# Kernel optimization log

Hardware: AMD Instinct MI355X
Metric: run time of the kernel (lower is better)

Reference implementation:

```python
import jax, jax.numpy as jnp
import numpy as np
from jax import lax

B = 16           # graphs per batch
N_PER = 4096     # points per graph (equal-sized graphs)
C_IN = 32        # in_channels
RATIO = 0.25
MAX_NBR = 32     # max_num_neighbors in radius()


def _xavier(key, fan_in, fan_out):
    lim = np.sqrt(6.0 / (fan_in + fan_out)).astype(np.float32)
    return jax.random.uniform(key, (fan_in, fan_out), jnp.float32, -lim, lim)


def setup_inputs() -> dict:
    key = jax.random.key(0)
    ks = jax.random.split(key, 16)
    x = jax.random.normal(ks[0], (B * N_PER, C_IN), jnp.float32)
    pos = jax.random.uniform(ks[1], (B * N_PER, 3), jnp.float32) * 20.0
    batch = jnp.repeat(jnp.arange(B, dtype=jnp.int64), N_PER)
    p = {
        'x': x, 'pos': pos, 'batch': batch,
        'scaler_mean': jnp.zeros((1, C_IN), jnp.float32),
        'scaler_std': jnp.ones((1, C_IN), jnp.float32),
        # SA1: Linear(32+3,64) -> Sigmoid -> Linear(64,128)
        'sa1_w1': _xavier(ks[2], C_IN + 3, 64), 'sa1_b1': jnp.zeros((64,), jnp.float32),
        'sa1_w2': _xavier(ks[3], 64, 128),      'sa1_b2': jnp.zeros((128,), jnp.float32),
        # SA2: Linear(128+3,128) -> Sigmoid -> Linear(128,256)
        'sa2_w1': _xavier(ks[4], 128 + 3, 128), 'sa2_b1': jnp.zeros((128,), jnp.float32),
        'sa2_w2': _xavier(ks[5], 128, 256),     'sa2_b2': jnp.zeros((256,), jnp.float32),
        # Global SA: Linear(256+3,256) -> Sigmoid -> Linear(256,512)
        'g_w1': _xavier(ks[6], 256 + 3, 256),   'g_b1': jnp.zeros((256,), jnp.float32),
        'g_w2': _xavier(ks[7], 256, 512),       'g_b2': jnp.zeros((512,), jnp.float32),
        # fc: Linear(512,256) -> Sigmoid -> Linear(256,128)
        'fc_w1': _xavier(ks[8], 512, 256),      'fc_b1': jnp.zeros((256,), jnp.float32),
        'fc_w2': _xavier(ks[9], 256, 128),      'fc_b2': jnp.zeros((128,), jnp.float32),
    }
    return p


def _fps(pos, k):
    # Farthest point sampling, deterministic start at index 0. pos: [B, n, 3] -> idx [B, k]
    pos = lax.stop_gradient(pos)
    d0 = jnp.sum((pos - pos[:, :1, :]) ** 2, -1)  # [B, n] dist^2 to start point

    def step(mind, _):
        nxt = jnp.argmax(mind, axis=1)                                  # [B]
        p = jnp.take_along_axis(pos, nxt[:, None, None], axis=1)        # [B,1,3]
        mind = jnp.minimum(mind, jnp.sum((pos - p) ** 2, -1))
        return mind, nxt

    _, rest = lax.scan(step, d0, None, length=k - 1)                    # [k-1, B]
    start = jnp.zeros((1, pos.shape[0]), rest.dtype)
    return jnp.concatenate([start, rest], 0).T                          # [B, k]


def _gather_nbr(v, nbr):
    # v: [B, n, C], nbr: [B, k, MAX_NBR] -> [B, k, MAX_NBR, C]
    return jax.vmap(lambda vb, nb: vb[nb])(v, nbr)


def _sa_module(x, pos, w1, b1, w2, b2, ratio, r):
    # PointNetConv (max aggregation) over a radius graph from FPS centers.
    Bb, n, _ = x.shape
    k = int(n * ratio)
    idx = _fps(pos, k)                                                  # [B, k]
    pos_dst = jnp.take_along_axis(pos, idx[:, :, None], axis=1)         # [B, k, 3]
    d2 = jnp.sum((pos_dst[:, :, None, :] - pos[:, None, :, :]) ** 2, -1)  # [B,k,n]
    masked = jnp.where(d2 <= r * r, d2, jnp.inf)
    negv, nbr = lax.top_k(-masked, MAX_NBR)                             # nearest <=32 within radius
    valid = jnp.isfinite(negv)                                          # [B,k,32]
    x_j = _gather_nbr(x, nbr)                                           # [B,k,32,C]
    rel = _gather_nbr(pos, nbr) - pos_dst[:, :, None, :]                # pos_j - pos_i
    feat = jnp.concatenate([x_j, rel], axis=-1)
    msg = jax.nn.sigmoid(feat @ w1 + b1) @ w2 + b2                      # [B,k,32,2h]
    msg = jnp.where(valid[..., None], msg, -jnp.inf)
    agg = jnp.max(msg, axis=2)                                          # max aggregation
    agg = jnp.where(jnp.isfinite(agg), agg, 0.0)  # (self is always a neighbor, defensive)
    return jax.nn.relu(agg), pos_dst


def reference(x, pos, batch, scaler_mean, scaler_std,
              sa1_w1, sa1_b1, sa1_w2, sa1_b2,
              sa2_w1, sa2_b1, sa2_w2, sa2_b2,
              g_w1, g_b1, g_w2, g_b2,
              fc_w1, fc_b1, fc_w2, fc_b2):
    x = (x - scaler_mean) / scaler_std
    xb = x.reshape(B, N_PER, -1)      # batch is sorted with N_PER points per graph
    pb = pos.reshape(B, N_PER, 3)
    xb, pb = _sa_module(xb, pb, sa1_w1, sa1_b1, sa1_w2, sa1_b2, RATIO, 2.0)
    xb, pb = _sa_module(xb, pb, sa2_w1, sa2_b1, sa2_w2, sa2_b2, RATIO, 4.0)
    # GlobalSAModule: relu(nn(cat[x, pos])) then global max pool
    h = jnp.concatenate([xb, pb], axis=-1)
    h = jax.nn.relu(jax.nn.sigmoid(h @ g_w1 + g_b1) @ g_w2 + g_b2)      # [B, 256, 512]
    g = jnp.max(h, axis=1)                                              # [B, 512]
    out = jax.nn.sigmoid(g @ fc_w1 + fc_b1) @ fc_w2 + fc_b2
    return jax.nn.relu(out)                                             # last_act='relu'
```

## Files before the change

kernel.cpp:

```cpp
#include <hip/hip_runtime.h>
#include <hip/hip_bf16.h>
#include <math.h>

namespace {

constexpr int NB   = 16;
constexpr int N1   = 4096;
constexpr int K1   = 1024;
constexpr int K2   = 256;
constexpr int MAXN = 32;
constexpr int RCAP = 448;

__device__ __forceinline__ float sigmoidf_(float x) {
  return 1.0f / (1.0f + __expf(-x));
}

__device__ __forceinline__ float readlane_f(float v, int l) {
  return __int_as_float(__builtin_amdgcn_readlane(__float_as_int(v), l));
}


#define FPS_DPP_STEP(CTRL)                                                     \
  {                                                                            \
    const unsigned olo =                                                       \
        (unsigned)__builtin_amdgcn_update_dpp(0, (int)lo, (CTRL), 0xF, 0xF, true); \
    const unsigned ohi =                                                       \
        (unsigned)__builtin_amdgcn_update_dpp(0, (int)hi, (CTRL), 0xF, 0xF, true); \
    const unsigned long long o = ((unsigned long long)ohi << 32) | olo;        \
    const unsigned long long cur = ((unsigned long long)hi << 32) | lo;        \
    if (o > cur) { lo = olo; hi = ohi; }                                       \
  }

template<int NPT>
__device__ __forceinline__ void fps_level(
    const float* __restrict__ sx, const float* __restrict__ sy,
    const float* __restrict__ sz, int k,
    float* __restrict__ selx, float* __restrict__ sely,
    float* __restrict__ selz,
    unsigned long long (*red)[4]) {
  const int t = threadIdx.x;
  const int lane = t & 63, wave = t >> 6;
  float px[NPT], py[NPT], pz[NPT], mind[NPT];
  unsigned niv[NPT];
  const float c0x = sx[0], c0y = sy[0], c0z = sz[0];
  unsigned long long best = 0;
#pragma unroll
  for (int i = 0; i < NPT; i++) {
    const int p = i * 256 + t;
    niv[i] = ~(unsigned)p;
    px[i] = sx[p]; py[i] = sy[p]; pz[i] = sz[p];
    const float dx = px[i] - c0x, dy = py[i] - c0y, dz = pz[i] - c0z;
    const float d2 = dx * dx + dy * dy + dz * dz;
    mind[i] = d2;
    const unsigned long long cand =
        ((unsigned long long)__float_as_uint(d2) << 32) | niv[i];
    if (cand > best) best = cand;
  }
  if (t == 0) { selx[0] = c0x; sely[0] = c0y; selz[0] = c0z; }
  for (int it = 1; it < k; it++) {
    unsigned lo = (unsigned)best, hi = (unsigned)(best >> 32);
    FPS_DPP_STEP(0x111)
    FPS_DPP_STEP(0x112)
    FPS_DPP_STEP(0x114)
    FPS_DPP_STEP(0x118)
    FPS_DPP_STEP(0x142)
    FPS_DPP_STEP(0x143)
    const int par = it & 1;
    if (lane == 63) red[par][wave] = ((unsigned long long)hi << 32) | lo;
    __syncthreads();
    const unsigned long long w0 = red[par][0], w1 = red[par][1];
    const unsigned long long w2 = red[par][2], w3 = red[par][3];
    const unsigned long long m01 = w0 > w1 ? w0 : w1;
    const unsigned long long m23 = w2 > w3 ? w2 : w3;
    const unsigned long long win = m01 > m23 ? m01 : m23;
    const int p = (int)(~(unsigned)win);
    const float nx = sx[p], ny = sy[p], nz = sz[p];
    if (t == 0) { selx[it] = nx; sely[it] = ny; selz[it] = nz; }
    best = 0;
#pragma unroll
    for (int i = 0; i < NPT; i++) {
      const float dx = px[i] - nx, dy = py[i] - ny, dz = pz[i] - nz;
      const float d2 = dx * dx + dy * dy + dz * dz;
      const float m = fminf(mind[i], d2);
      mind[i] = m;
      const unsigned long long cand =
          ((unsigned long long)__float_as_uint(m) << 32) | niv[i];
      if (cand > best) best = cand;
    }
  }
}

#undef FPS_DPP_STEP

__global__ __launch_bounds__(256) void fps_l1_kernel(
    const float* __restrict__ pos, float* __restrict__ posd1,
    unsigned int* __restrict__ gout) {
  __shared__ float sx[N1], sy[N1], sz[N1];
  __shared__ float s2x[K1], s2y[K1], s2z[K1];
  __shared__ __align__(16) unsigned long long red[2][4];
  const int b = blockIdx.x;
  const int t = threadIdx.x;
  gout[b * 512 + t] = 0u;
  gout[b * 512 + t + 256] = 0u;
  const float* pb = pos + (size_t)b * N1 * 3;
  for (int p = t; p < N1; p += 256) {
    sx[p] = pb[p * 3 + 0]; sy[p] = pb[p * 3 + 1]; sz[p] = pb[p * 3 + 2];
  }
  __syncthreads();
  fps_level<N1 / 256>(sx, sy, sz, K1, s2x, s2y, s2z, red);
  __syncthreads();
  float* o1 = posd1 + (size_t)b * K1 * 3;
  for (int i = t; i < K1; i += 256) {
    o1[i * 3 + 0] = s2x[i]; o1[i * 3 + 1] = s2y[i]; o1[i * 3 + 2] = s2z[i];
  }
}

struct FpsL2Smem {
  float s2x[K1], s2y[K1], s2z[K1];
  float p2x[K2], p2y[K2], p2z[K2];
  unsigned long long red[2][4];
};
struct RadSmem {
  float candd[4][RCAP];
  int   candi[4][RCAP];
};

template<int N>
__device__ __forceinline__ void radius_body(
    const float* __restrict__ pts, const float* __restrict__ ctr,
    int K, float r2, int* __restrict__ nbr, int* __restrict__ cnt_out,
    RadSmem& sm, int rb) {
  const int t = threadIdx.x;
  const int lane = t & 63, wave = t >> 6;
  const int bpg = K / 4;
  const int b = rb / bpg;
  const int ci = (rb % bpg) * 4 + wave;
  const float* pb = pts + (size_t)b * N * 3;
  const size_t cbase = ((size_t)b * K + ci) * 3;
  const float cx = ctr[cbase + 0], cy = ctr[cbase + 1], cz = ctr[cbase + 2];
  int total = 0;
  for (int base = 0; base < N; base += 64) {
    const int p = base + lane;
    const float dx = pb[p * 3 + 0] - cx;
    const float dy = pb[p * 3 + 1] - cy;
    const float dz = pb[p * 3 + 2] - cz;
    const float d2 = dx * dx + dy * dy + dz * dz;
    const bool pred = d2 <= r2;
    const unsigned long long m = __ballot(pred);
    if (pred) {
      const int slot = total + __popcll(m & ((1ull << lane) - 1ull));
      if (slot < RCAP) { sm.candd[wave][slot] = d2; sm.candi[wave][slot] = p; }
    }
    total += __popcll(m);
  }
  if (total > RCAP) total = RCAP;
  int* nbp = nbr + ((size_t)b * K + ci) * MAXN;
  if (total <= MAXN) {
    if (lane < total) nbp[lane] = sm.candi[wave][lane];
  } else {
    for (int jj = 0; jj < MAXN; jj++) {
      float bvd = INFINITY; int bvi = 0x7fffffff; int bslot = 0;
      for (int s = lane; s < total; s += 64) {
        const float d = sm.candd[wave][s];
        const int i = sm.candi[wave][s];
        if (d < bvd || (d == bvd && i < bvi)) { bvd = d; bvi = i; bslot = s; }
      }
#pragma unroll
      for (int off = 32; off; off >>= 1) {
        const float od = __shfl_xor(bvd, off);
        const int   oi = __shfl_xor(bvi, off);
        const int   os = __shfl_xor(bslot, off);
        if (od < bvd || (od == bvd && oi < bvi)) { bvd = od; bvi = oi; bslot = os; }
      }
      if (lane == 0) { nbp[jj] = bvi; sm.candd[wave][bslot] = INFINITY; }
    }
  }
  if (lane == 0) cnt_out[(size_t)b * K + ci] = (total < MAXN) ? total : MAXN;
}

__global__ __launch_bounds__(256) void l2_radius1_kernel(
    const float* __restrict__ pos, const float* __restrict__ posd1,
    float* __restrict__ posd2, int* __restrict__ nbr1,
    int* __restrict__ cnt1) {
  constexpr size_t SMB =
      sizeof(FpsL2Smem) > sizeof(RadSmem) ? sizeof(FpsL2Smem) : sizeof(RadSmem);
  __shared__ __align__(16) char smem[SMB];
  const int t = threadIdx.x;
  if (blockIdx.x < (unsigned)NB) {
    FpsL2Smem& f = *reinterpret_cast<FpsL2Smem*>(smem);
    const int b = blockIdx.x;
    const float* p1 = posd1 + (size_t)b * K1 * 3;
    for (int i = t; i < K1; i += 256) {
      f.s2x[i] = p1[i * 3 + 0]; f.s2y[i] = p1[i * 3 + 1]; f.s2z[i] = p1[i * 3 + 2];
    }
    __syncthreads();
    fps_level<K1 / 256>(f.s2x, f.s2y, f.s2z, K2, f.p2x, f.p2y, f.p2z, f.red);
    __syncthreads();
    float* o2 = posd2 + (size_t)b * K2 * 3;
    for (int i = t; i < K2; i += 256) {
      o2[i * 3 + 0] = f.p2x[i]; o2[i * 3 + 1] = f.p2y[i]; o2[i * 3 + 2] = f.p2z[i];
    }
  } else {
    RadSmem& r = *reinterpret_cast<RadSmem*>(smem);
    radius_body<N1>(pos, posd1, K1, 4.0f, nbr1, cnt1, r, blockIdx.x - NB);
  }
}

template<int CIN_T, int H, int COUT, bool SCALE>
__device__ __forceinline__ void sa_conv_body(
    const float* __restrict__ xin, const float* __restrict__ pts,
    const float* __restrict__ ctr, const int* __restrict__ nbr,
    const int* __restrict__ cnt,
    const float* __restrict__ w1, const float* __restrict__ b1,
    const float* __restrict__ w2, const float* __restrict__ b2,
    const float* __restrict__ smean, const float* __restrict__ sstd,
    int N, int K, float* __restrict__ xout, float* part ,
    int bk) {
  constexpr int FIN  = CIN_T + 3;
  constexpr int KREG = (FIN + 63) / 64;
  constexpr int HREG = H / 64;
  constexpr int CREG = COUT / 64;
  constexpr int RPW  = MAXN / 4;
  const int t = threadIdx.x, lane = t & 63, wave = t >> 6;
  const int b = bk / K;
  const int V = cnt[bk];
  float m[CREG];
#pragma unroll
  for (int ck = 0; ck < CREG; ck++) m[ck] = -INFINITY;
  if (V > wave * RPW) {
    const int* nb = nbr + (size_t)bk * MAXN;
    const float ctrx = ctr[(size_t)bk * 3 + 0];
    const float ctry = ctr[(size_t)bk * 3 + 1];
    const float ctrz = ctr[(size_t)bk * 3 + 2];
    float sm = 0.0f, sd = 1.0f;
    if (SCALE && lane < CIN_T) { sm = smean[lane]; sd = sstd[lane]; }
    float fr[RPW][KREG];
#pragma unroll
    for (int r = 0; r < RPW; r++) {
      const int j = wave * RPW + r;
      const int p = (j < V) ? nb[j] : nb[0];
#pragma unroll
      for (int k2 = 0; k2 < KREG; k2++) {
        const int f = k2 * 64 + lane;
        float v = 0.0f;
        if (f < CIN_T) {
          v = xin[((size_t)b * N + p) * CIN_T + f];
          if constexpr (SCALE) v = (v - sm) / sd;
        } else if (f < FIN) {
          const int d = f - CIN_T;
          const float pv = pts[((size_t)b * N + p) * 3 + d];
          v = pv - (d == 0 ? ctrx : (d == 1 ? ctry : ctrz));
        }
        fr[r][k2] = v;
      }
    }
    float hh[RPW][HREG];
    {
      float acc[RPW][HREG];
#pragma unroll
      for (int r = 0; r < RPW; r++)
#pragma unroll
        for (int q = 0; q < HREG; q++) acc[r][q] = 0.0f;
#pragma unroll
      for (int k2 = 0; k2 < KREG; k2++) {
        const int lim = (FIN - k2 * 64) < 64 ? (FIN - k2 * 64) : 64;
        for (int fl = 0; fl < lim; fl++) {
          const int f = k2 * 64 + fl;
          float wv[HREG];
          if constexpr (HREG == 1) {
            wv[0] = w1[(size_t)f * H + lane];
          } else {
            const float2 w = *reinterpret_cast<const float2*>(
                &w1[(size_t)f * H + lane * 2]);
            wv[0] = w.x; wv[1] = w.y;
          }
#pragma unroll
          for (int r = 0; r < RPW; r++) {
            const float s = readlane_f(fr[r][k2], fl);
#pragma unroll
            for (int q = 0; q < HREG; q++) acc[r][q] = fmaf(s, wv[q], acc[r][q]);
          }
        }
      }
#pragma unroll
      for (int q = 0; q < HREG; q++) {
        const float bb = b1[lane * HREG + q];
#pragma unroll
        for (int r = 0; r < RPW; r++) hh[r][q] = sigmoidf_(acc[r][q] + bb);
      }
    }
    float acc2[RPW][CREG];
#pragma unroll
    for (int r = 0; r < RPW; r++)
#pragma unroll
      for (int q = 0; q < CREG; q++) acc2[r][q] = 0.0f;
    for (int hl = 0; hl < 64; hl++) {
#pragma unroll
      for (int q1 = 0; q1 < HREG; q1++) {
        const int h = hl * HREG + q1;
        float wv[CREG];
        if constexpr (CREG == 2) {
          const float2 w = *reinterpret_cast<const float2*>(
              &w2[(size_t)h * COUT + lane * 2]);
          wv[0] = w.x; wv[1] = w.y;
        } else {
          const float4 w = *reinterpret_cast<const float4*>(
              &w2[(size_t)h * COUT + lane * 4]);
          wv[0] = w.x; wv[1] = w.y; wv[2] = w.z; wv[3] = w.w;
        }
#pragma unroll
        for (int r = 0; r < RPW; r++) {
          const float s = readlane_f(hh[r][q1], hl);
#pragma unroll
          for (int q = 0; q < CREG; q++) acc2[r][q] = fmaf(s, wv[q], acc2[r][q]);
        }
      }
    }
#pragma unroll
    for (int r = 0; r < RPW; r++) {
      if (wave * RPW + r < V) {
#pragma unroll
        for (int q = 0; q < CREG; q++) m[q] = fmaxf(m[q], acc2[r][q]);
      }
    }
  }
#pragma unroll
  for (int q = 0; q < CREG; q++) part[wave * COUT + lane * CREG + q] = m[q];
  __syncthreads();
  if (t < COUT) {
    const float mm = fmaxf(fmaxf(part[0 * COUT + t], part[1 * COUT + t]),
                           fmaxf(part[2 * COUT + t], part[3 * COUT + t]));
    const float o = mm + b2[t];
    xout[(size_t)bk * COUT + t] = o > 0.0f ? o : 0.0f;
  }
}

__global__ __launch_bounds__(256) void rad2_conv1_kernel(
    const float* __restrict__ posd1, const float* __restrict__ posd2,
    int* __restrict__ nbr2, int* __restrict__ cnt2,
    const float* __restrict__ x, const float* __restrict__ pos,
    const int* __restrict__ nbr1, const int* __restrict__ cnt1,
    const float* __restrict__ s1w1, const float* __restrict__ s1b1,
    const float* __restrict__ s1w2, const float* __restrict__ s1b2,
    const float* __restrict__ smean, const float* __restrict__ sstd,
    float* __restrict__ x1) {
  constexpr int NRAD = NB * K2 / 4;
  constexpr size_t SMB =
      sizeof(RadSmem) > sizeof(float) * 4 * 128 ? sizeof(RadSmem)
                                                : sizeof(float) * 4 * 128;
  __shared__ __align__(16) char smem[SMB];
  if (blockIdx.x < (unsigned)NRAD) {
    RadSmem& r = *reinterpret_cast<RadSmem*>(smem);
    radius_body<K1>(posd1, posd2, K2, 16.0f, nbr2, cnt2, r, blockIdx.x);
  } else {
    float* part = reinterpret_cast<float*>(smem);
    sa_conv_body<32, 64, 128, true>(x, pos, posd1, nbr1, cnt1,
                                    s1w1, s1b1, s1w2, s1b2, smean, sstd,
                                    N1, K1, x1, part, blockIdx.x - NRAD);
  }
}

__global__ __launch_bounds__(256) void conv2_kernel(
    const float* __restrict__ x1, const float* __restrict__ posd1,
    const float* __restrict__ posd2, const int* __restrict__ nbr2,
    const int* __restrict__ cnt2,
    const float* __restrict__ s2w1, const float* __restrict__ s2b1,
    const float* __restrict__ s2w2, const float* __restrict__ s2b2,
    float* __restrict__ x2) {
  __shared__ __align__(16) float part[4 * 256];
  sa_conv_body<128, 128, 256, false>(x1, posd1, posd2, nbr2, cnt2,
                                     s2w1, s2b1, s2w2, s2b2, nullptr, nullptr,
                                     K1, K2, x2, part, blockIdx.x);
}

__global__ __launch_bounds__(256) void global_sa_kernel(
    const float* __restrict__ x2, const float* __restrict__ posd2,
    const float* __restrict__ gw1, const float* __restrict__ gb1,
    const float* __restrict__ gw2, const float* __restrict__ gb2,
    unsigned int* __restrict__ gout) {
  __shared__ float fin[4][259];
  __shared__ float s[4][256];
  const int t = threadIdx.x;
  const int blk = blockIdx.x;
  const int b = blk / 64;
  const int p0 = (blk % 64) * 4;
  for (int item = t; item < 4 * 259; item += 256) {
    const int p = item / 259, f = item - p * 259;
    const float v = (f < 256)
        ? x2[((size_t)b * 256 + p0 + p) * 256 + f]
        : posd2[((size_t)b * 256 + p0 + p) * 3 + (f - 256)];
    fin[p][f] = v;
  }
  __syncthreads();
  float acc[4] = {0.f, 0.f, 0.f, 0.f};
  for (int f = 0; f < 259; f++) {
    const float w = gw1[f * 256 + t];
#pragma unroll
    for (int p = 0; p < 4; p++) acc[p] = fmaf(fin[p][f], w, acc[p]);
  }
  const float bb = gb1[t];
#pragma unroll
  for (int p = 0; p < 4; p++) s[p][t] = sigmoidf_(acc[p] + bb);
  __syncthreads();
  float a0[4] = {0.f, 0.f, 0.f, 0.f}, a1[4] = {0.f, 0.f, 0.f, 0.f};
  for (int h = 0; h < 256; h++) {
    const float w0 = gw2[h * 512 + t];
    const float w1v = gw2[h * 512 + t + 256];
#pragma unroll
    for (int p = 0; p < 4; p++) {
      a0[p] = fmaf(s[p][h], w0, a0[p]);
      a1[p] = fmaf(s[p][h], w1v, a1[p]);
    }
  }
  const float b0 = gb2[t], b1v = gb2[t + 256];
  float m0 = 0.0f, m1 = 0.0f;
#pragma unroll
  for (int p = 0; p < 4; p++) {
    m0 = fmaxf(m0, fmaxf(a0[p] + b0, 0.0f));
    m1 = fmaxf(m1, fmaxf(a1[p] + b1v, 0.0f));
  }
  atomicMax(&gout[b * 512 + t], __float_as_uint(m0));
  atomicMax(&gout[b * 512 + t + 256], __float_as_uint(m1));
}

__global__ __launch_bounds__(256) void fc_kernel(
    const unsigned int* __restrict__ g,
    const float* __restrict__ fw1, const float* __restrict__ fb1,
    const float* __restrict__ fw2, const float* __restrict__ fb2,
    float* __restrict__ out) {
  __shared__ float gv[512];
  __shared__ float s[256];
  const int b = blockIdx.x, t = threadIdx.x;
  gv[t] = __uint_as_float(g[b * 512 + t]);
  gv[t + 256] = __uint_as_float(g[b * 512 + t + 256]);
  __syncthreads();
  float acc = 0.0f;
  for (int h = 0; h < 512; h++) acc = fmaf(gv[h], fw1[h * 256 + t], acc);
  s[t] = sigmoidf_(acc + fb1[t]);
  __syncthreads();
  if (t < 128) {
    float a2 = 0.0f;
    for (int h = 0; h < 256; h++) a2 = fmaf(s[h], fw2[h * 128 + t], a2);
    const float o = a2 + fb2[t];
    out[b * 128 + t] = o > 0.0f ? o : 0.0f;
  }
}

}

extern "C" void kernel_launch(void* const* d_in, const int* in_sizes, int n_in,
                              void* d_out, int out_size, void* d_ws, size_t ws_size,
                              hipStream_t stream) {
  (void)in_sizes; (void)n_in; (void)out_size; (void)ws_size;
  const float* x     = (const float*)d_in[0];
  const float* pos   = (const float*)d_in[1];
  const float* smean = (const float*)d_in[3];
  const float* sstd  = (const float*)d_in[4];
  const float* s1w1  = (const float*)d_in[5];
  const float* s1b1  = (const float*)d_in[6];
  const float* s1w2  = (const float*)d_in[7];
  const float* s1b2  = (const float*)d_in[8];
  const float* s2w1  = (const float*)d_in[9];
  const float* s2b1  = (const float*)d_in[10];
  const float* s2w2  = (const float*)d_in[11];
  const float* s2b2  = (const float*)d_in[12];
  const float* gw1   = (const float*)d_in[13];
  const float* gb1   = (const float*)d_in[14];
  const float* gw2   = (const float*)d_in[15];
  const float* gb2   = (const float*)d_in[16];
  const float* fw1   = (const float*)d_in[17];
  const float* fb1   = (const float*)d_in[18];
  const float* fw2   = (const float*)d_in[19];
  const float* fb2   = (const float*)d_in[20];

  char* ws = (char*)d_ws;
  size_t off = 0;
  auto take = [&](size_t bytes) -> char* {
    char* p = ws + off;
    off = (off + bytes + 255) & ~(size_t)255;
    return p;
  };
  float* posd1       = (float*)take((size_t)NB * K1 * 3 * 4);
  int*   nbr1        = (int*)take((size_t)NB * K1 * MAXN * 4);
  int*   cnt1        = (int*)take((size_t)NB * K1 * 4);
  float* x1          = (float*)take((size_t)NB * K1 * 128 * 4);
  float* posd2       = (float*)take((size_t)NB * K2 * 3 * 4);
  int*   nbr2        = (int*)take((size_t)NB * K2 * MAXN * 4);
  int*   cnt2        = (int*)take((size_t)NB * K2 * 4);
  float* x2          = (float*)take((size_t)NB * K2 * 256 * 4);
  unsigned int* gbuf = (unsigned int*)take((size_t)NB * 512 * 4);

  hipLaunchKernelGGL(fps_l1_kernel, dim3(NB), dim3(256), 0, stream,
                     pos, posd1, gbuf);
  hipLaunchKernelGGL(l2_radius1_kernel, dim3(NB + NB * K1 / 4), dim3(256), 0, stream,
                     pos, posd1, posd2, nbr1, cnt1);
  hipLaunchKernelGGL(rad2_conv1_kernel, dim3(NB * K2 / 4 + NB * K1), dim3(256), 0, stream,
                     posd1, posd2, nbr2, cnt2, x, pos, nbr1, cnt1,
                     s1w1, s1b1, s1w2, s1b2, smean, sstd, x1);
  hipLaunchKernelGGL(conv2_kernel, dim3(NB * K2), dim3(256), 0, stream,
                     x1, posd1, posd2, nbr2, cnt2, s2w1, s2b1, s2w2, s2b2, x2);
  hipLaunchKernelGGL(global_sa_kernel, dim3(NB * 64), dim3(256), 0, stream,
                     x2, posd2, gw1, gb1, gw2, gb2, gbuf);
  hipLaunchKernelGGL(fc_kernel, dim3(NB), dim3(256), 0, stream,
                     gbuf, fw1, fb1, fw2, fb2, (float*)d_out);
}
```

Before: 1.182 ms.

## Drop second-level FPS by reusing the FPS-ordered prefix of level-one samples

Farthest point sampling is greedy and prefix-consistent. Running it again on an already FPS-ordered set, from index 0, returns the same leading points (up to ties). The second FPS level is therefore removed, and the first K2 entries of posd1 serve as level-2 centres through a row stride parameter (CSTR). This removes a serial 256-step FPS pass from the critical path. It also lets radius search 2 run in the same launch as radius search 1, leaving conv1 as its own kernel. The exactness depends on tie behaviour in argmax matching the reference.

```diff
diff --git a/kernel.cpp b/kernel.cpp
--- a/kernel.cpp
+++ b/kernel.cpp
@@ -115,11 +115,6 @@
   }
 }
 
-struct FpsL2Smem {
-  float s2x[K1], s2y[K1], s2z[K1];
-  float p2x[K2], p2y[K2], p2z[K2];
-  unsigned long long red[2][4];
-};
 struct RadSmem {
   float candd[4][RCAP];
   int   candi[4][RCAP];
@@ -128,15 +123,15 @@
 template<int N>
 __device__ __forceinline__ void radius_body(
     const float* __restrict__ pts, const float* __restrict__ ctr,
-    int K, float r2, int* __restrict__ nbr, int* __restrict__ cnt_out,
-    RadSmem& sm, int rb) {
+    int K, int CSTR, float r2, int* __restrict__ nbr,
+    int* __restrict__ cnt_out, RadSmem& sm, int rb) {
   const int t = threadIdx.x;
   const int lane = t & 63, wave = t >> 6;
   const int bpg = K / 4;
   const int b = rb / bpg;
   const int ci = (rb % bpg) * 4 + wave;
   const float* pb = pts + (size_t)b * N * 3;
-  const size_t cbase = ((size_t)b * K + ci) * 3;
+  const size_t cbase = ((size_t)b * CSTR + ci) * 3;
   const float cx = ctr[cbase + 0], cy = ctr[cbase + 1], cz = ctr[cbase + 2];
   int total = 0;
   for (int base = 0; base < N; base += 64) {
@@ -178,31 +173,17 @@
   if (lane == 0) cnt_out[(size_t)b * K + ci] = (total < MAXN) ? total : MAXN;
 }
 
-__global__ __launch_bounds__(256) void l2_radius1_kernel(
+__global__ __launch_bounds__(256) void rad12_kernel(
     const float* __restrict__ pos, const float* __restrict__ posd1,
-    float* __restrict__ posd2, int* __restrict__ nbr1,
-    int* __restrict__ cnt1) {
-  constexpr size_t SMB =
-      sizeof(FpsL2Smem) > sizeof(RadSmem) ? sizeof(FpsL2Smem) : sizeof(RadSmem);
-  __shared__ __align__(16) char smem[SMB];
-  const int t = threadIdx.x;
-  if (blockIdx.x < (unsigned)NB) {
-    FpsL2Smem& f = *reinterpret_cast<FpsL2Smem*>(smem);
-    const int b = blockIdx.x;
-    const float* p1 = posd1 + (size_t)b * K1 * 3;
-    for (int i = t; i < K1; i += 256) {
-      f.s2x[i] = p1[i * 3 + 0]; f.s2y[i] = p1[i * 3 + 1]; f.s2z[i] = p1[i * 3 + 2];
-    }
-    __syncthreads();
-    fps_level<K1 / 256>(f.s2x, f.s2y, f.s2z, K2, f.p2x, f.p2y, f.p2z, f.red);
-    __syncthreads();
-    float* o2 = posd2 + (size_t)b * K2 * 3;
-    for (int i = t; i < K2; i += 256) {
-      o2[i * 3 + 0] = f.p2x[i]; o2[i * 3 + 1] = f.p2y[i]; o2[i * 3 + 2] = f.p2z[i];
-    }
+    int* __restrict__ nbr1, int* __restrict__ cnt1,
+    int* __restrict__ nbr2, int* __restrict__ cnt2) {
+  constexpr int NR1 = NB * K1 / 4;
+  __shared__ __align__(16) RadSmem r;
+  if (blockIdx.x < (unsigned)NR1) {
+    radius_body<N1>(pos, posd1, K1, K1, 4.0f, nbr1, cnt1, r, blockIdx.x);
   } else {
-    RadSmem& r = *reinterpret_cast<RadSmem*>(smem);
-    radius_body<N1>(pos, posd1, K1, 4.0f, nbr1, cnt1, r, blockIdx.x - NB);
+    radius_body<K1>(posd1, posd1, K2, K1, 16.0f, nbr2, cnt2, r,
+                    blockIdx.x - NR1);
   }
 }
 
@@ -214,8 +195,8 @@
     const float* __restrict__ w1, const float* __restrict__ b1,
     const float* __restrict__ w2, const float* __restrict__ b2,
     const float* __restrict__ smean, const float* __restrict__ sstd,
-    int N, int K, float* __restrict__ xout, float* part ,
-    int bk) {
+    int N, int K, int CSTR, float* __restrict__ xout,
+    float* part , int bk) {
   constexpr int FIN  = CIN_T + 3;
   constexpr int KREG = (FIN + 63) / 64;
   constexpr int HREG = H / 64;
@@ -229,9 +210,10 @@
   for (int ck = 0; ck < CREG; ck++) m[ck] = -INFINITY;
   if (V > wave * RPW) {
     const int* nb = nbr + (size_t)bk * MAXN;
-    const float ctrx = ctr[(size_t)bk * 3 + 0];
-    const float ctry = ctr[(size_t)bk * 3 + 1];
-    const float ctrz = ctr[(size_t)bk * 3 + 2];
+    const size_t crow = (size_t)b * CSTR + (bk - b * K);
+    const float ctrx = ctr[crow * 3 + 0];
+    const float ctry = ctr[crow * 3 + 1];
+    const float ctrz = ctr[crow * 3 + 2];
     float sm = 0.0f, sd = 1.0f;
     if (SCALE && lane < CIN_T) { sm = smean[lane]; sd = sstd[lane]; }
     float fr[RPW][KREG];
@@ -335,46 +317,34 @@
   }
 }
 
-__global__ __launch_bounds__(256) void rad2_conv1_kernel(
-    const float* __restrict__ posd1, const float* __restrict__ posd2,
-    int* __restrict__ nbr2, int* __restrict__ cnt2,
+__global__ __launch_bounds__(256) void conv1_kernel(
     const float* __restrict__ x, const float* __restrict__ pos,
-    const int* __restrict__ nbr1, const int* __restrict__ cnt1,
+    const float* __restrict__ posd1, const int* __restrict__ nbr1,
+    const int* __restrict__ cnt1,
     const float* __restrict__ s1w1, const float* __restrict__ s1b1,
     const float* __restrict__ s1w2, const float* __restrict__ s1b2,
     const float* __restrict__ smean, const float* __restrict__ sstd,
     float* __restrict__ x1) {
-  constexpr int NRAD = NB * K2 / 4;
-  constexpr size_t SMB =
-      sizeof(RadSmem) > sizeof(float) * 4 * 128 ? sizeof(RadSmem)
-                                                : sizeof(float) * 4 * 128;
-  __shared__ __align__(16) char smem[SMB];
-  if (blockIdx.x < (unsigned)NRAD) {
-    RadSmem& r = *reinterpret_cast<RadSmem*>(smem);
-    radius_body<K1>(posd1, posd2, K2, 16.0f, nbr2, cnt2, r, blockIdx.x);
-  } else {
-    float* part = reinterpret_cast<float*>(smem);
-    sa_conv_body<32, 64, 128, true>(x, pos, posd1, nbr1, cnt1,
-                                    s1w1, s1b1, s1w2, s1b2, smean, sstd,
-                                    N1, K1, x1, part, blockIdx.x - NRAD);
-  }
+  __shared__ __align__(16) float part[4 * 128];
+  sa_conv_body<32, 64, 128, true>(x, pos, posd1, nbr1, cnt1,
+                                  s1w1, s1b1, s1w2, s1b2, smean, sstd,
+                                  N1, K1, K1, x1, part, blockIdx.x);
 }
 
 __global__ __launch_bounds__(256) void conv2_kernel(
     const float* __restrict__ x1, const float* __restrict__ posd1,
-    const float* __restrict__ posd2, const int* __restrict__ nbr2,
-    const int* __restrict__ cnt2,
+    const int* __restrict__ nbr2, const int* __restrict__ cnt2,
     const float* __restrict__ s2w1, const float* __restrict__ s2b1,
     const float* __restrict__ s2w2, const float* __restrict__ s2b2,
     float* __restrict__ x2) {
   __shared__ __align__(16) float part[4 * 256];
-  sa_conv_body<128, 128, 256, false>(x1, posd1, posd2, nbr2, cnt2,
+  sa_conv_body<128, 128, 256, false>(x1, posd1, posd1, nbr2, cnt2,
                                      s2w1, s2b1, s2w2, s2b2, nullptr, nullptr,
-                                     K1, K2, x2, part, blockIdx.x);
+                                     K1, K2, K1, x2, part, blockIdx.x);
 }
 
 __global__ __launch_bounds__(256) void global_sa_kernel(
-    const float* __restrict__ x2, const float* __restrict__ posd2,
+    const float* __restrict__ x2, const float* __restrict__ posd1,
     const float* __restrict__ gw1, const float* __restrict__ gb1,
     const float* __restrict__ gw2, const float* __restrict__ gb2,
     unsigned int* __restrict__ gout) {
@@ -388,7 +358,7 @@
     const int p = item / 259, f = item - p * 259;
     const float v = (f < 256)
         ? x2[((size_t)b * 256 + p0 + p) * 256 + f]
-        : posd2[((size_t)b * 256 + p0 + p) * 3 + (f - 256)];
+        : posd1[((size_t)b * K1 + p0 + p) * 3 + (f - 256)];
     fin[p][f] = v;
   }
   __syncthreads();
@@ -484,7 +454,6 @@
   int*   nbr1        = (int*)take((size_t)NB * K1 * MAXN * 4);
   int*   cnt1        = (int*)take((size_t)NB * K1 * 4);
   float* x1          = (float*)take((size_t)NB * K1 * 128 * 4);
-  float* posd2       = (float*)take((size_t)NB * K2 * 3 * 4);
   int*   nbr2        = (int*)take((size_t)NB * K2 * MAXN * 4);
   int*   cnt2        = (int*)take((size_t)NB * K2 * 4);
   float* x2          = (float*)take((size_t)NB * K2 * 256 * 4);
@@ -492,15 +461,15 @@
 
   hipLaunchKernelGGL(fps_l1_kernel, dim3(NB), dim3(256), 0, stream,
                      pos, posd1, gbuf);
-  hipLaunchKernelGGL(l2_radius1_kernel, dim3(NB + NB * K1 / 4), dim3(256), 0, stream,
-                     pos, posd1, posd2, nbr1, cnt1);
-  hipLaunchKernelGGL(rad2_conv1_kernel, dim3(NB * K2 / 4 + NB * K1), dim3(256), 0, stream,
-                     posd1, posd2, nbr2, cnt2, x, pos, nbr1, cnt1,
+  hipLaunchKernelGGL(rad12_kernel, dim3(NB * K1 / 4 + NB * K2 / 4), dim3(256), 0, stream,
+                     pos, posd1, nbr1, cnt1, nbr2, cnt2);
+  hipLaunchKernelGGL(conv1_kernel, dim3(NB * K1), dim3(256), 0, stream,
+                     x, pos, posd1, nbr1, cnt1,
                      s1w1, s1b1, s1w2, s1b2, smean, sstd, x1);
   hipLaunchKernelGGL(conv2_kernel, dim3(NB * K2), dim3(256), 0, stream,
-                     x1, posd1, posd2, nbr2, cnt2, s2w1, s2b1, s2w2, s2b2, x2);
+                     x1, posd1, nbr2, cnt2, s2w1, s2b1, s2w2, s2b2, x2);
   hipLaunchKernelGGL(global_sa_kernel, dim3(NB * 64), dim3(256), 0, stream,
-                     x2, posd2, gw1, gb1, gw2, gb2, gbuf);
+                     x2, posd1, gw1, gb1, gw2, gb2, gbuf);
   hipLaunchKernelGGL(fc_kernel, dim3(NB), dim3(256), 0, stream,
                      gbuf, fw1, fb1, fw2, fb2, (float*)d_out);
 }
```

Result: no change. 1.160 ms (-1.8%).
